# Performance work log

Measured on AMD Instinct MI355X. Metric: run time of the kernel, lower is better.

Reference implementation:

```python
import jax, jax.numpy as jnp
import numpy as np

N_NODES = 50000
N_EDGES = 800000
DIM = 128
LN_EPS = 1e-5


def setup_inputs() -> dict:
    key = jax.random.key(0)
    k1, k2, k3, k4, k5 = jax.random.split(key, 5)
    x = jax.random.normal(k1, (N_NODES, DIM), dtype=jnp.float32)
    edge_index = jax.random.randint(k2, (2, N_EDGES), 0, N_NODES, dtype=jnp.int64)
    edge_weight = jax.random.uniform(k3, (N_EDGES,), dtype=jnp.float32)
    # GCNConv linear (PyG Linear: out = x @ W.T + b)
    W = jax.random.normal(k4, (DIM, DIM), dtype=jnp.float32) / np.sqrt(DIM)
    b = jnp.zeros((DIM,), dtype=jnp.float32)
    # pygnn.LayerNorm(dim, mode='node') affine params
    ln_weight = jnp.ones((DIM,), dtype=jnp.float32)
    ln_bias = jnp.zeros((DIM,), dtype=jnp.float32)
    return {"x": x, "edge_index": edge_index, "edge_weight": edge_weight,
            "W": W, "b": b, "ln_weight": ln_weight, "ln_bias": ln_bias}


def reference(x, edge_index, edge_weight, W, b, ln_weight, ln_bias):
    n = x.shape[0]
    # --- LayerNorm (mode='node'): per-node over feature dim ---
    mu = jnp.mean(x, axis=-1, keepdims=True)
    var = jnp.mean(jnp.square(x - mu), axis=-1, keepdims=True)
    xn = (x - mu) * jax.lax.rsqrt(var + LN_EPS) * ln_weight + ln_bias
    # --- GCNConv: linear first, then normalized propagate ---
    h = xn @ W.T  # [N, dim]
    row, col = edge_index[0], edge_index[1]  # source, target
    # add self loops (fill_value = 1.0)
    loop = jnp.arange(n, dtype=edge_index.dtype)
    row_f = jnp.concatenate([row, loop])
    col_f = jnp.concatenate([col, loop])
    ew_f = jnp.concatenate([edge_weight, jnp.ones((n,), dtype=edge_weight.dtype)])
    # symmetric gcn normalization: deg over target (col)
    deg = jax.ops.segment_sum(ew_f, col_f, num_segments=n)
    dinv = jnp.where(deg > 0, jax.lax.rsqrt(deg), 0.0)
    norm = dinv[row_f] * ew_f * dinv[col_f]  # [E+N]
    # gather-scale-scatter
    msg = h[row_f] * norm[:, None]  # [E+N, dim]
    out = jax.ops.segment_sum(msg, col_f, num_segments=n) + b
    # --- GELU (torch default = exact erf form); dropout is identity (p=0 / eval) ---
    return jax.nn.gelu(out, approximate=False)
```

## Files before the change

### kernel.cpp

```cpp
#include <hip/hip_runtime.h>
#include <math.h>

#define DIM 128
#define LN_EPS 1e-5f
#define HB 512
#define CAP 2048

typedef __attribute__((ext_vector_type(8))) short short8;
typedef __attribute__((ext_vector_type(4))) float floatx4;

__device__ __forceinline__ float gelu_exact(float v) {
    return 0.5f * v * (1.0f + erff(v * 0.70710678118654752f));
}
__device__ __forceinline__ float bf2f(unsigned short u) {
    return __uint_as_float(((unsigned)u) << 16);
}
__device__ __forceinline__ short f2bf(float f) {
    unsigned b = __float_as_uint(f);
    return (short)((b + 0x7FFF + ((b >> 16) & 1)) >> 16);
}

__global__ __launch_bounds__(256) void gemm_hist_kernel(
    const float* __restrict__ x, const float* __restrict__ W,
    const float* __restrict__ lnw, const float* __restrict__ lnb,
    unsigned short* __restrict__ h16,
    const int* __restrict__ col, int* __restrict__ hist,
    int n, int E, int nbkt)
{
    __shared__ short swb[2048 * 8];
    __shared__ short axb[1024 * 8];
    const int tid = threadIdx.x;

    if ((int)blockIdx.x < HB) {
        int* lh = (int*)swb;
        for (int b = tid; b < nbkt; b += 256) lh[b] = 0;
        __syncthreads();
        int g = blockIdx.x;
        int chunk = (E + HB - 1) / HB;
        int e0 = g * chunk;
        int e1 = e0 + chunk; if (e1 > E) e1 = E;
        for (int e = e0 + tid; e < e1; e += 256)
            atomicAdd(&lh[col[e] >> 6], 1);
        __syncthreads();
        for (int b = tid; b < nbkt; b += 256)
            hist[(size_t)g * nbkt + b] = lh[b];
        return;
    }

    const int gb = blockIdx.x - HB;
    const int n0 = gb * 64;

    for (int c = tid; c < 2048; c += 256) {
        int nrow = ((c >> 8) << 4) | (c & 15);
        int kb   = (((c >> 6) & 3) << 5) + (((c >> 4) & 3) << 3);
        const float* wp = W + nrow * DIM + kb;
        float4 w0 = *(const float4*)wp;
        float4 w1 = *(const float4*)(wp + 4);
        short8 p;
        p[0] = f2bf(w0.x); p[1] = f2bf(w0.y); p[2] = f2bf(w0.z); p[3] = f2bf(w0.w);
        p[4] = f2bf(w1.x); p[5] = f2bf(w1.y); p[6] = f2bf(w1.z); p[7] = f2bf(w1.w);
        *(short8*)&swb[c * 8] = p;
    }

    {
        int m = tid >> 2, sub = tid & 3;
        int node = n0 + m;
        bool valid = (node < n);
        const float4* xp = (const float4*)(x + (size_t)node * DIM + sub * 32);
        float4 v[8];
        float s = 0.f, ss = 0.f;
        #pragma unroll
        for (int i = 0; i < 8; ++i) {
            v[i] = valid ? xp[i] : make_float4(0.f, 0.f, 0.f, 0.f);
            s  += v[i].x + v[i].y + v[i].z + v[i].w;
            ss += v[i].x * v[i].x + v[i].y * v[i].y + v[i].z * v[i].z + v[i].w * v[i].w;
        }
        s += __shfl_xor(s, 1); ss += __shfl_xor(ss, 1);
        s += __shfl_xor(s, 2); ss += __shfl_xor(ss, 2);
        float mu   = s * (1.0f / 128.0f);
        float var  = ss * (1.0f / 128.0f) - mu * mu;
        float rstd = rsqrtf(var + LN_EPS);

        int mt = m >> 4, mloc = m & 15;
        #pragma unroll
        for (int quad = 0; quad < 4; ++quad) {
            float4 a = v[2 * quad], c4 = v[2 * quad + 1];
            const float4* lw = (const float4*)(lnw + sub * 32 + quad * 8);
            const float4* lb = (const float4*)(lnb + sub * 32 + quad * 8);
            float4 lw0 = lw[0], lw1 = lw[1], lb0 = lb[0], lb1 = lb[1];
            short8 p;
            p[0] = f2bf((a.x  - mu) * rstd * lw0.x + lb0.x);
            p[1] = f2bf((a.y  - mu) * rstd * lw0.y + lb0.y);
            p[2] = f2bf((a.z  - mu) * rstd * lw0.z + lb0.z);
            p[3] = f2bf((a.w  - mu) * rstd * lw0.w + lb0.w);
            p[4] = f2bf((c4.x - mu) * rstd * lw1.x + lb1.x);
            p[5] = f2bf((c4.y - mu) * rstd * lw1.y + lb1.y);
            p[6] = f2bf((c4.z - mu) * rstd * lw1.z + lb1.z);
            p[7] = f2bf((c4.w - mu) * rstd * lw1.w + lb1.w);
            int slot = mt * 256 + sub * 64 + quad * 16 + mloc;
            *(short8*)&axb[slot * 8] = p;
        }
    }
    __syncthreads();

    const int w    = tid >> 6;
    const int lane = tid & 63;

    short8 afrag[4];
    #pragma unroll
    for (int kq = 0; kq < 4; ++kq)
        afrag[kq] = *(const short8*)&axb[(w * 256 + kq * 64 + lane) * 8];

    floatx4 acc[8];
    #pragma unroll
    for (int jt = 0; jt < 8; ++jt) acc[jt] = (floatx4){0.f, 0.f, 0.f, 0.f};

    #pragma unroll
    for (int jt = 0; jt < 8; ++jt) {
        #pragma unroll
        for (int kq = 0; kq < 4; ++kq) {
            short8 bfrag = *(const short8*)&swb[(jt * 256 + kq * 64 + lane) * 8];
            acc[jt] = __builtin_amdgcn_mfma_f32_16x16x32_bf16(afrag[kq], bfrag,
                                                              acc[jt], 0, 0, 0);
        }
    }

    const int quad = lane >> 4, nl = lane & 15;
    #pragma unroll
    for (int jt = 0; jt < 8; ++jt) {
        #pragma unroll
        for (int r = 0; r < 4; ++r) {
            int rnode = n0 + w * 16 + quad * 4 + r;
            if (rnode < n)
                h16[(size_t)rnode * DIM + jt * 16 + nl] = (unsigned short)f2bf(acc[jt][r]);
        }
    }
}

__global__ __launch_bounds__(256) void expand_kernel(
    const int* __restrict__ hist, int* __restrict__ base,
    int* __restrict__ cnt, int nbkt)
{
    __shared__ int ls[256];
    const int tid = threadIdx.x;
    const int b = blockIdx.x;

    int v0 = hist[(size_t)(2 * tid)     * nbkt + b];
    int v1 = hist[(size_t)(2 * tid + 1) * nbkt + b];
    int p = v0 + v1;
    ls[tid] = p;
    __syncthreads();
    int inc = p;
    for (int off = 1; off < 256; off <<= 1) {
        int add = (tid >= off) ? ls[tid - off] : 0;
        __syncthreads();
        inc += add;
        ls[tid] = inc;
        __syncthreads();
    }
    int ex = inc - p;
    int a0 = b * CAP + ex;
    base[(size_t)(2 * tid)     * nbkt + b] = a0;
    base[(size_t)(2 * tid + 1) * nbkt + b] = a0 + v0;
    if (tid == 255) cnt[b] = inc;
}

__global__ __launch_bounds__(256) void bucket_scatter_kernel(
    const int* __restrict__ row, const int* __restrict__ col,
    const float* __restrict__ ew, const int* __restrict__ base,
    int2* __restrict__ srt, int E, int nbkt)
{
    __shared__ int cur[1024];
    const int tid = threadIdx.x, g = blockIdx.x;
    for (int b = tid; b < nbkt; b += 256)
        cur[b] = base[(size_t)g * nbkt + b];
    __syncthreads();
    int chunk = (E + HB - 1) / HB;
    int e0 = g * chunk;
    int e1 = e0 + chunk; if (e1 > E) e1 = E;
    for (int e = e0 + tid; e < e1; e += 256) {
        int c = col[e];
        int pos = atomicAdd(&cur[c >> 6], 1);
        srt[pos] = make_int2(((c & 63) << 16) | row[e], __float_as_int(ew[e]));
    }
}

__global__ __launch_bounds__(256) void dinv_kernel(
    const int2* __restrict__ srt, const int* __restrict__ cnt,
    float* __restrict__ dinv, int n)
{
    __shared__ float w64[64];
    const int tid = threadIdx.x, b = blockIdx.x;
    if (tid < 64) w64[tid] = 0.f;
    __syncthreads();
    int c = cnt[b];
    int s0 = b * CAP;
    for (int i = tid; i < c; i += 256) {
        int2 v = srt[s0 + i];
        atomicAdd(&w64[(v.x >> 16) & 63], __int_as_float(v.y));
    }
    __syncthreads();
    if (tid < 64)
        dinv[b * 64 + tid] = rsqrtf(1.0f + w64[tid]);
}

__global__ __launch_bounds__(256) void bucket_gather_kernel(
    const int2* __restrict__ srt, const int* __restrict__ cnt,
    const float* __restrict__ dinv, const unsigned short* __restrict__ h16,
    const float* __restrict__ bias, float* __restrict__ out, int n)
{
    __shared__ int2  bufA[CAP];
    __shared__ int2  bufB[CAP];
    __shared__ int   k64[64], off64[64], cur64[64];
    __shared__ float di64[64];
    const int tid = threadIdx.x, b = blockIdx.x;

    if (tid < 64) { k64[tid] = 0; di64[tid] = dinv[b * 64 + tid]; }
    __syncthreads();

    const int c  = cnt[b];
    const int s0 = b * CAP;
    const int grp = tid >> 4;
    const int sub = tid & 15;

    if (c <= CAP) {
        for (int i = tid; i < c; i += 256) {
            int2 v = srt[s0 + i];
            bufA[i] = v;
            atomicAdd(&k64[(v.x >> 16) & 63], 1);
        }
        __syncthreads();
        if (tid == 0) {
            int run = 0;
            #pragma unroll
            for (int d = 0; d < 64; ++d) { off64[d] = run; cur64[d] = run; run += k64[d]; }
        }
        __syncthreads();
        for (int i = tid; i < c; i += 256) {
            int2 v = bufA[i];
            int d   = (v.x >> 16) & 63;
            int src = v.x & 0xFFFF;
            float nrm = dinv[src] * __int_as_float(v.y) * di64[d];
            int p = atomicAdd(&cur64[d], 1);
            bufB[p] = make_int2(src, __float_as_int(nrm));
        }
        __syncthreads();

        #pragma unroll
        for (int dd = 0; dd < 4; ++dd) {
            int d = dd * 16 + grp;
            int dest = b * 64 + d;
            if (dest >= n) continue;
            float di = di64[d];
            short8 sv = *(const short8*)(h16 + (size_t)dest * DIM + sub * 8);
            float s2 = di * di;
            float acc[8];
            #pragma unroll
            for (int k = 0; k < 8; ++k) acc[k] = s2 * bf2f((unsigned short)sv[k]);

            int j  = off64[d];
            int je = j + k64[d];
            for (; j + 3 < je; j += 4) {
                int2 e0 = bufB[j],     e1 = bufB[j + 1];
                int2 e2 = bufB[j + 2], e3 = bufB[j + 3];
                short8 a0 = *(const short8*)(h16 + (size_t)e0.x * DIM + sub * 8);
                short8 a1 = *(const short8*)(h16 + (size_t)e1.x * DIM + sub * 8);
                short8 a2 = *(const short8*)(h16 + (size_t)e2.x * DIM + sub * 8);
                short8 a3 = *(const short8*)(h16 + (size_t)e3.x * DIM + sub * 8);
                float n0 = __int_as_float(e0.y);
                float n1 = __int_as_float(e1.y);
                float n2 = __int_as_float(e2.y);
                float n3 = __int_as_float(e3.y);
                #pragma unroll
                for (int k = 0; k < 8; ++k) {
                    acc[k] = fmaf(n0, bf2f((unsigned short)a0[k]), acc[k]);
                    acc[k] = fmaf(n1, bf2f((unsigned short)a1[k]), acc[k]);
                    acc[k] = fmaf(n2, bf2f((unsigned short)a2[k]), acc[k]);
                    acc[k] = fmaf(n3, bf2f((unsigned short)a3[k]), acc[k]);
                }
            }
            for (; j < je; ++j) {
                int2 e0 = bufB[j];
                float n0 = __int_as_float(e0.y);
                short8 a = *(const short8*)(h16 + (size_t)e0.x * DIM + sub * 8);
                #pragma unroll
                for (int k = 0; k < 8; ++k)
                    acc[k] = fmaf(n0, bf2f((unsigned short)a[k]), acc[k]);
            }

            float4 b0 = *(const float4*)(bias + sub * 8);
            float4 b1 = *(const float4*)(bias + sub * 8 + 4);
            float4 o0, o1;
            o0.x = gelu_exact(acc[0] + b0.x); o0.y = gelu_exact(acc[1] + b0.y);
            o0.z = gelu_exact(acc[2] + b0.z); o0.w = gelu_exact(acc[3] + b0.w);
            o1.x = gelu_exact(acc[4] + b1.x); o1.y = gelu_exact(acc[5] + b1.y);
            o1.z = gelu_exact(acc[6] + b1.z); o1.w = gelu_exact(acc[7] + b1.w);
            float* op = out + (size_t)dest * DIM + sub * 8;
            *(float4*)op       = o0;
            *(float4*)(op + 4) = o1;
        }
    } else {
        #pragma unroll
        for (int dd = 0; dd < 4; ++dd) {
            int d = dd * 16 + grp;
            int dest = b * 64 + d;
            if (dest >= n) continue;
            float di = di64[d];
            short8 sv = *(const short8*)(h16 + (size_t)dest * DIM + sub * 8);
            float s2 = di * di;
            float acc[8];
            #pragma unroll
            for (int k = 0; k < 8; ++k) acc[k] = s2 * bf2f((unsigned short)sv[k]);
            for (int i = 0; i < c; ++i) {
                int2 v = srt[s0 + i];
                if (((v.x >> 16) & 63) != d) continue;
                int src = v.x & 0xFFFF;
                float nrm = dinv[src] * __int_as_float(v.y) * di;
                short8 a = *(const short8*)(h16 + (size_t)src * DIM + sub * 8);
                #pragma unroll
                for (int k = 0; k < 8; ++k)
                    acc[k] = fmaf(nrm, bf2f((unsigned short)a[k]), acc[k]);
            }
            float4 b0 = *(const float4*)(bias + sub * 8);
            float4 b1 = *(const float4*)(bias + sub * 8 + 4);
            float4 o0, o1;
            o0.x = gelu_exact(acc[0] + b0.x); o0.y = gelu_exact(acc[1] + b0.y);
            o0.z = gelu_exact(acc[2] + b0.z); o0.w = gelu_exact(acc[3] + b0.w);
            o1.x = gelu_exact(acc[4] + b1.x); o1.y = gelu_exact(acc[5] + b1.y);
            o1.z = gelu_exact(acc[6] + b1.z); o1.w = gelu_exact(acc[7] + b1.w);
            float* op = out + (size_t)dest * DIM + sub * 8;
            *(float4*)op       = o0;
            *(float4*)(op + 4) = o1;
        }
    }
}

extern "C" void kernel_launch(void* const* d_in, const int* in_sizes, int n_in,
                              void* d_out, int out_size, void* d_ws, size_t ws_size,
                              hipStream_t stream)
{
    const float* x    = (const float*)d_in[0];
    const int*   ei   = (const int*)d_in[1];
    const float* ew   = (const float*)d_in[2];
    const float* W    = (const float*)d_in[3];
    const float* b    = (const float*)d_in[4];
    const float* ln_w = (const float*)d_in[5];
    const float* ln_b = (const float*)d_in[6];
    float* out = (float*)d_out;

    const int n = in_sizes[0] / DIM;
    const int E = in_sizes[2];
    const int* row  = ei;
    const int* colp = ei + E;
    const int nbkt = (n + 63) / 64;

    int2*           srt  = (int2*)d_ws;
    unsigned short* h16  = (unsigned short*)(srt + (size_t)nbkt * CAP);
    int*            hist = (int*)(h16 + (size_t)n * DIM);
    int*            base = hist + (size_t)HB * nbkt;
    int*            cnt  = base + (size_t)HB * nbkt;
    float*          dinv = (float*)(cnt + nbkt);

    const int GB = (n + 63) / 64;

    gemm_hist_kernel<<<HB + GB, 256, 0, stream>>>(x, W, ln_w, ln_b, h16,
                                                  colp, hist, n, E, nbkt);
    expand_kernel<<<nbkt, 256, 0, stream>>>(hist, base, cnt, nbkt);
    bucket_scatter_kernel<<<HB, 256, 0, stream>>>(row, colp, ew, base, srt, E, nbkt);
    dinv_kernel<<<nbkt, 256, 0, stream>>>(srt, cnt, dinv, n);
    bucket_gather_kernel<<<nbkt, 256, 0, stream>>>(srt, cnt, dinv, h16, b, out, n);
}
```

Measured before the change: 171.0 us.

## Locally sort edge chunks in LDS before bucket scatter; stage GEMM output

The bucket scatter now reduces the number of edge-chunk blocks to 128. Each block counts and prefix-sums its edges per bucket in LDS, places them into a shared buffer sorted by bucket, and then writes contiguous runs to global memory, so stores are coalesced instead of scattered per edge. The GEMM epilogue stages bf16 results through LDS so each node row is written with wide vector stores. The per-bucket offset computation in the gather kernel changes from a serial loop on one thread to a wave shuffle scan. Risks: fewer blocks in the histogram and scatter phases reduce parallelism, the large LDS footprint limits occupancy, and the row index packing assumes n fits in 16 bits.

```diff
diff --git a/kernel.cpp b/kernel.cpp
--- a/kernel.cpp
+++ b/kernel.cpp
@@ -3,8 +3,9 @@
 
 #define DIM 128
 #define LN_EPS 1e-5f
-#define HB 512
+#define HB 128
 #define CAP 2048
+#define SBUF 6400
 
 typedef __attribute__((ext_vector_type(8))) short short8;
 typedef __attribute__((ext_vector_type(4))) float floatx4;
@@ -28,11 +29,11 @@
     int n, int E, int nbkt)
 {
     __shared__ short swb[2048 * 8];
-    __shared__ short axb[1024 * 8];
+    __shared__ short ubuf[8448];
     const int tid = threadIdx.x;
 
     if ((int)blockIdx.x < HB) {
-        int* lh = (int*)swb;
+        int* lh = (int*)ubuf;
         for (int b = tid; b < nbkt; b += 256) lh[b] = 0;
         __syncthreads();
         int g = blockIdx.x;
@@ -49,6 +50,7 @@
 
     const int gb = blockIdx.x - HB;
     const int n0 = gb * 64;
+    short* axb = ubuf;
 
     for (int c = tid; c < 2048; c += 256) {
         int nrow = ((c >> 8) << 4) | (c & 15);
@@ -110,6 +112,7 @@
     #pragma unroll
     for (int kq = 0; kq < 4; ++kq)
         afrag[kq] = *(const short8*)&axb[(w * 256 + kq * 64 + lane) * 8];
+    __syncthreads();
 
     floatx4 acc[8];
     #pragma unroll
@@ -126,13 +129,23 @@
     }
 
     const int quad = lane >> 4, nl = lane & 15;
+    const int HS = 132;
+    short* hb = ubuf;
     #pragma unroll
     for (int jt = 0; jt < 8; ++jt) {
         #pragma unroll
-        for (int r = 0; r < 4; ++r) {
-            int rnode = n0 + w * 16 + quad * 4 + r;
-            if (rnode < n)
-                h16[(size_t)rnode * DIM + jt * 16 + nl] = (unsigned short)f2bf(acc[jt][r]);
+        for (int r = 0; r < 4; ++r)
+            hb[(w * 16 + quad * 4 + r) * HS + jt * 16 + nl] = f2bf(acc[jt][r]);
+    }
+    __syncthreads();
+    {
+        int rrow = tid >> 2, seg = tid & 3;
+        int node = n0 + rrow;
+        if (node < n) {
+            const short8* sp = (const short8*)&hb[rrow * HS + seg * 32];
+            short8 v0 = sp[0], v1 = sp[1], v2 = sp[2], v3 = sp[3];
+            short8* dp = (short8*)(h16 + (size_t)node * DIM + seg * 32);
+            dp[0] = v0; dp[1] = v1; dp[2] = v2; dp[3] = v3;
         }
     }
 }
@@ -145,12 +158,10 @@
     const int tid = threadIdx.x;
     const int b = blockIdx.x;
 
-    int v0 = hist[(size_t)(2 * tid)     * nbkt + b];
-    int v1 = hist[(size_t)(2 * tid + 1) * nbkt + b];
-    int p = v0 + v1;
-    ls[tid] = p;
-    __syncthreads();
-    int inc = p;
+    int v = (tid < HB) ? hist[(size_t)tid * nbkt + b] : 0;
+    ls[tid] = v;
+    __syncthreads();
+    int inc = v;
     for (int off = 1; off < 256; off <<= 1) {
         int add = (tid >= off) ? ls[tid - off] : 0;
         __syncthreads();
@@ -158,30 +169,76 @@
         ls[tid] = inc;
         __syncthreads();
     }
-    int ex = inc - p;
-    int a0 = b * CAP + ex;
-    base[(size_t)(2 * tid)     * nbkt + b] = a0;
-    base[(size_t)(2 * tid + 1) * nbkt + b] = a0 + v0;
+    if (tid < HB) base[(size_t)tid * nbkt + b] = b * CAP + (inc - v);
     if (tid == 255) cnt[b] = inc;
 }
 
-__global__ __launch_bounds__(256) void bucket_scatter_kernel(
+__global__ __launch_bounds__(256) void scatter_sort_kernel(
     const int* __restrict__ row, const int* __restrict__ col,
     const float* __restrict__ ew, const int* __restrict__ base,
     int2* __restrict__ srt, int E, int nbkt)
 {
-    __shared__ int cur[1024];
+    __shared__ int2 sbuf[SBUF];
+    __shared__ int  lofs[1024];
+    __shared__ int  cur[1024];
+    __shared__ int  ls[256];
     const int tid = threadIdx.x, g = blockIdx.x;
-    for (int b = tid; b < nbkt; b += 256)
-        cur[b] = base[(size_t)g * nbkt + b];
-    __syncthreads();
-    int chunk = (E + HB - 1) / HB;
-    int e0 = g * chunk;
+    const int chunk = (E + HB - 1) / HB;
+    const int e0 = g * chunk;
     int e1 = e0 + chunk; if (e1 > E) e1 = E;
-    for (int e = e0 + tid; e < e1; e += 256) {
-        int c = col[e];
-        int pos = atomicAdd(&cur[c >> 6], 1);
-        srt[pos] = make_int2(((c & 63) << 16) | row[e], __float_as_int(ew[e]));
+    const int cntT = e1 - e0;
+    const int nq = (nbkt + 255) / 256;
+
+    if (cntT <= SBUF) {
+        for (int b = tid; b < nbkt; b += 256) cur[b] = 0;
+        __syncthreads();
+        for (int e = e0 + tid; e < e1; e += 256)
+            atomicAdd(&cur[col[e] >> 6], 1);
+        __syncthreads();
+        int carry = 0;
+        for (int qq = 0; qq < nq; ++qq) {
+            int b = qq * 256 + tid;
+            int v = (b < nbkt) ? cur[b] : 0;
+            __syncthreads();
+            ls[tid] = v;
+            __syncthreads();
+            int inc = v;
+            for (int off = 1; off < 256; off <<= 1) {
+                int add = (tid >= off) ? ls[tid - off] : 0;
+                __syncthreads();
+                inc += add;
+                ls[tid] = inc;
+                __syncthreads();
+            }
+            if (b < nbkt) lofs[b] = carry + inc - v;
+            carry += ls[255];
+        }
+        __syncthreads();
+        for (int b = tid; b < nbkt; b += 256) cur[b] = lofs[b];
+        __syncthreads();
+        for (int e = e0 + tid; e < e1; e += 256) {
+            int c = col[e];
+            int b = c >> 6;
+            int p = atomicAdd(&cur[b], 1);
+            sbuf[p] = make_int2((b << 22) | ((c & 63) << 16) | row[e],
+                                __float_as_int(ew[e]));
+        }
+        __syncthreads();
+        for (int b = tid; b < nbkt; b += 256) cur[b] = base[(size_t)g * nbkt + b];
+        __syncthreads();
+        for (int i = tid; i < cntT; i += 256) {
+            int2 v = sbuf[i];
+            int b = ((unsigned)v.x) >> 22;
+            srt[cur[b] + (i - lofs[b])] = make_int2(v.x & 0x3FFFFF, v.y);
+        }
+    } else {
+        for (int b = tid; b < nbkt; b += 256) cur[b] = base[(size_t)g * nbkt + b];
+        __syncthreads();
+        for (int e = e0 + tid; e < e1; e += 256) {
+            int c = col[e];
+            int pos = atomicAdd(&cur[c >> 6], 1);
+            srt[pos] = make_int2(((c & 63) << 16) | row[e], __float_as_int(ew[e]));
+        }
     }
 }
 
@@ -230,10 +287,16 @@
             atomicAdd(&k64[(v.x >> 16) & 63], 1);
         }
         __syncthreads();
-        if (tid == 0) {
-            int run = 0;
+        if (tid < 64) {
+            int v = k64[tid];
+            int inc = v;
             #pragma unroll
-            for (int d = 0; d < 64; ++d) { off64[d] = run; cur64[d] = run; run += k64[d]; }
+            for (int off = 1; off < 64; off <<= 1) {
+                int t = __shfl_up(inc, off, 64);
+                if (tid >= off) inc += t;
+            }
+            off64[tid] = inc - v;
+            cur64[tid] = inc - v;
         }
         __syncthreads();
         for (int i = tid; i < c; i += 256) {
@@ -366,7 +429,7 @@
     gemm_hist_kernel<<<HB + GB, 256, 0, stream>>>(x, W, ln_w, ln_b, h16,
                                                   colp, hist, n, E, nbkt);
     expand_kernel<<<nbkt, 256, 0, stream>>>(hist, base, cnt, nbkt);
-    bucket_scatter_kernel<<<HB, 256, 0, stream>>>(row, colp, ew, base, srt, E, nbkt);
+    scatter_sort_kernel<<<HB, 256, 0, stream>>>(row, colp, ew, base, srt, E, nbkt);
     dinv_kernel<<<nbkt, 256, 0, stream>>>(srt, cnt, dinv, n);
     bucket_gather_kernel<<<nbkt, 256, 0, stream>>>(srt, cnt, dinv, h16, b, out, n);
 }
```

After: 192.9 us. 1.13x slower.
